# Kernel tuning notes

Hardware: AMD Instinct MI355X
Metric: run time of the kernel (lower is better)

The kernel has to match this reference:

```python
import jax, jax.numpy as jnp
import numpy as np

GAMMA = 1.0
B = 2_000_000
P = 10  # prototype_count


def setup_inputs() -> dict:
    key = jax.random.key(0)
    ks = jax.random.split(key, 17)

    def w(k, shape, scale=0.2):
        return (jax.random.normal(k, shape, dtype=jnp.float32) * scale)

    return {
        "inputs": jax.random.normal(ks[0], (B, 8), dtype=jnp.float32),
        # feature_map: Linear(8,16)
        "W_fm": w(ks[1], (8, 16)), "b_fm": w(ks[2], (16,)),
        # conv1: Linear(16,16)
        "W1": w(ks[3], (16, 16)), "b1": w(ks[4], (16,)),
        # pool1: Linear(16,12)
        "Wp1": w(ks[5], (16, 12)), "bp1": w(ks[6], (12,)),
        # conv2: Linear(12,8)
        "W2": w(ks[7], (12, 8)), "b2": w(ks[8], (8,)),
        # pool2: Linear(8,4)
        "Wp2": w(ks[9], (8, 4)), "bp2": w(ks[10], (4,)),
        # conv3: Linear(4,4)
        "W3": w(ks[11], (4, 4)), "b3": w(ks[12], (4,)),
        # prototypes in conv3 output space [P,4]
        "prototypes": jax.random.normal(ks[13], (P, 4), dtype=jnp.float32),
        # head: Linear(4+P, 1)
        "Wh": w(ks[14], (4 + P, 1)), "bh": w(ks[15], (1,)),
    }


def reference(inputs, W_fm, b_fm, W1, b1, Wp1, bp1, W2, b2, Wp2, bp2,
              W3, b3, prototypes, Wh, bh):
    # Tanh-MLP stack: 8 -> 16 -> 16 -> 12 -> 8 -> 4 -> 4
    x = jnp.tanh(inputs @ W_fm + b_fm)
    x = jnp.tanh(x @ W1 + b1)
    x = jnp.tanh(x @ Wp1 + bp1)
    x = jnp.tanh(x @ W2 + b2)
    x = jnp.tanh(x @ Wp2 + bp2)
    x = jnp.tanh(x @ W3 + b3)                      # [B, 4]
    # Vectorized RBF kernel vs prototype set (replaces per-sample Python loop):
    # ||x_i - p_j||^2 = ||x_i||^2 + ||p_j||^2 - 2 x_i . p_j
    x2 = jnp.sum(x * x, axis=-1, keepdims=True)    # [B, 1]
    p2 = jnp.sum(prototypes * prototypes, axis=-1) # [P]
    d2 = x2 + p2[None, :] - 2.0 * (x @ prototypes.T)  # [B, P]
    kernel_features = jnp.exp(-GAMMA * d2)         # [B, P]
    combined = jnp.concatenate([x, kernel_features], axis=1)  # [B, 4+P]
    return jax.nn.sigmoid(combined @ Wh + bh)      # [B, 1]
```

## Files before the change

### kernel.cpp

```cpp
#include <hip/hip_runtime.h>

#define THREADS 256
typedef float v2f __attribute__((ext_vector_type(2)));

__device__ __forceinline__ v2f tanh2(v2f x) {
    v2f xs = x * 2.885390081777927f;
    v2f e  = { __builtin_amdgcn_exp2f(xs.x),
               __builtin_amdgcn_exp2f(xs.y) };
    v2f ep = e + 1.0f;
    v2f r  = { __builtin_amdgcn_rcpf(ep.x),
               __builtin_amdgcn_rcpf(ep.y) };
    return (v2f){-2.0f, -2.0f} * r + 1.0f;
}

template<int IN, int OUT>
__device__ __forceinline__ void dense(const float* x, float* y,
                                      const float* __restrict__ W,
                                      const float* __restrict__ b) {
#pragma unroll
    for (int j = 0; j < OUT; j += 2) {
        v2f acc = { b[j], b[j + 1] };
#pragma unroll
        for (int k = 0; k < IN; ++k) {
            v2f w = { W[k * OUT + j], W[k * OUT + j + 1] };
            acc += w * x[k];
        }
        v2f t = tanh2(acc);
        y[j] = t.x; y[j + 1] = t.y;
    }
}

__global__ __launch_bounds__(THREADS) void qcnn_fused(
        const float* __restrict__ inputs,
        const float* __restrict__ W_fm, const float* __restrict__ b_fm,
        const float* __restrict__ W1,  const float* __restrict__ b1,
        const float* __restrict__ Wp1, const float* __restrict__ bp1,
        const float* __restrict__ W2,  const float* __restrict__ b2,
        const float* __restrict__ Wp2, const float* __restrict__ bp2,
        const float* __restrict__ W3,  const float* __restrict__ b3,
        const float* __restrict__ protos,
        const float* __restrict__ Wh,  const float* __restrict__ bh,
        float* __restrict__ out, int B) {
    const int tid = blockIdx.x * THREADS + threadIdx.x;
    if (tid >= B) return;

    float xa[16], xb[16];

    const float4* in4 = reinterpret_cast<const float4*>(inputs) + (size_t)tid * 2;
    float4 v0 = in4[0], v1 = in4[1];
    xa[0] = v0.x; xa[1] = v0.y; xa[2] = v0.z; xa[3] = v0.w;
    xa[4] = v1.x; xa[5] = v1.y; xa[6] = v1.z; xa[7] = v1.w;

    dense<8, 16>(xa, xb, W_fm, b_fm);
    dense<16, 16>(xb, xa, W1, b1);
    dense<16, 12>(xa, xb, Wp1, bp1);
    dense<12, 8>(xb, xa, W2, b2);
    dense<8, 4>(xa, xb, Wp2, bp2);
    dense<4, 4>(xb, xa, W3, b3);

    v2f ha = { bh[0], 0.0f };
    ha += (v2f){ xa[0], xa[1] } * (v2f){ Wh[0], Wh[1] };
    ha += (v2f){ xa[2], xa[3] } * (v2f){ Wh[2], Wh[3] };
    float acc = ha.x + ha.y;

#pragma unroll
    for (int j = 0; j < 10; j += 2) {
        v2f d2 = { 0.0f, 0.0f };
#pragma unroll
        for (int k = 0; k < 4; ++k) {
            v2f p = { protos[j * 4 + k], protos[(j + 1) * 4 + k] };
            v2f d = (v2f){ xa[k], xa[k] } - p;
            d2 += d * d;
        }
        v2f d2s = d2 * -1.4426950408889634f;
        float kf0 = __builtin_amdgcn_exp2f(d2s.x);
        float kf1 = __builtin_amdgcn_exp2f(d2s.y);
        acc = fmaf(kf0, Wh[4 + j], acc);
        acc = fmaf(kf1, Wh[5 + j], acc);
    }
    float e = __builtin_amdgcn_exp2f(acc * -1.4426950408889634f);
    out[tid] = __builtin_amdgcn_rcpf(1.0f + e);
}

extern "C" void kernel_launch(void* const* d_in, const int* in_sizes, int n_in,
                              void* d_out, int out_size, void* d_ws, size_t ws_size,
                              hipStream_t stream) {
    const float* inputs = (const float*)d_in[0];
    float* out = (float*)d_out;
    const int B = in_sizes[0] / 8;
    const int blocks = (B + THREADS - 1) / THREADS;
    qcnn_fused<<<blocks, THREADS, 0, stream>>>(
        inputs,
        (const float*)d_in[1],  (const float*)d_in[2],
        (const float*)d_in[3],  (const float*)d_in[4],
        (const float*)d_in[5],  (const float*)d_in[6],
        (const float*)d_in[7],  (const float*)d_in[8],
        (const float*)d_in[9],  (const float*)d_in[10],
        (const float*)d_in[11], (const float*)d_in[12],
        (const float*)d_in[13],
        (const float*)d_in[14], (const float*)d_in[15],
        out, B);
}
```

Before: 53.11 us.

## Process two samples per thread with packed v2f lanes across samples

Each thread now handles two batch rows (t0 and t0+gridDim*THREADS), packing the two samples into v2f lanes so every dense layer, the RBF distances and the head use packed FMA with scalar weights broadcast. The grid is halved and launch bounds request 4 waves per EU. The aim is to amortize the uniform weight loads and keep packed math fully used without pairing output columns. In exchange each thread needs more registers and has fewer threads in flight to hide memory latency.

```diff
diff --git a/kernel.cpp b/kernel.cpp
--- a/kernel.cpp
+++ b/kernel.cpp
@@ -14,23 +14,20 @@
 }
 
 template<int IN, int OUT>
-__device__ __forceinline__ void dense(const float* x, float* y,
+__device__ __forceinline__ void dense(const v2f* x, v2f* y,
                                       const float* __restrict__ W,
                                       const float* __restrict__ b) {
 #pragma unroll
-    for (int j = 0; j < OUT; j += 2) {
-        v2f acc = { b[j], b[j + 1] };
+    for (int j = 0; j < OUT; ++j) {
+        v2f acc = { b[j], b[j] };
 #pragma unroll
-        for (int k = 0; k < IN; ++k) {
-            v2f w = { W[k * OUT + j], W[k * OUT + j + 1] };
-            acc += w * x[k];
-        }
-        v2f t = tanh2(acc);
-        y[j] = t.x; y[j + 1] = t.y;
+        for (int k = 0; k < IN; ++k)
+            acc += x[k] * W[k * OUT + j];
+        y[j] = tanh2(acc);
     }
 }
 
-__global__ __launch_bounds__(THREADS) void qcnn_fused(
+__global__ __launch_bounds__(THREADS, 4) void qcnn_fused(
         const float* __restrict__ inputs,
         const float* __restrict__ W_fm, const float* __restrict__ b_fm,
         const float* __restrict__ W1,  const float* __restrict__ b1,
@@ -41,15 +38,21 @@
         const float* __restrict__ protos,
         const float* __restrict__ Wh,  const float* __restrict__ bh,
         float* __restrict__ out, int B) {
-    const int tid = blockIdx.x * THREADS + threadIdx.x;
-    if (tid >= B) return;
+    const int t0 = blockIdx.x * THREADS + threadIdx.x;
+    const int T  = gridDim.x * THREADS;
+    const int iA = t0, iB = t0 + T;
+    const bool vA = iA < B, vB = iB < B;
 
-    float xa[16], xb[16];
-
-    const float4* in4 = reinterpret_cast<const float4*>(inputs) + (size_t)tid * 2;
-    float4 v0 = in4[0], v1 = in4[1];
-    xa[0] = v0.x; xa[1] = v0.y; xa[2] = v0.z; xa[3] = v0.w;
-    xa[4] = v1.x; xa[5] = v1.y; xa[6] = v1.z; xa[7] = v1.w;
+    v2f xa[16], xb[16];
+    {
+        const float4* pa = reinterpret_cast<const float4*>(inputs) + (size_t)(vA ? iA : 0) * 2;
+        const float4* pb = reinterpret_cast<const float4*>(inputs) + (size_t)(vB ? iB : 0) * 2;
+        float4 a0 = pa[0], a1 = pa[1], b0 = pb[0], b1 = pb[1];
+        xa[0] = (v2f){a0.x, b0.x}; xa[1] = (v2f){a0.y, b0.y};
+        xa[2] = (v2f){a0.z, b0.z}; xa[3] = (v2f){a0.w, b0.w};
+        xa[4] = (v2f){a1.x, b1.x}; xa[5] = (v2f){a1.y, b1.y};
+        xa[6] = (v2f){a1.z, b1.z}; xa[7] = (v2f){a1.w, b1.w};
+    }
 
     dense<8, 16>(xa, xb, W_fm, b_fm);
     dense<16, 16>(xb, xa, W1, b1);
@@ -58,28 +61,27 @@
     dense<8, 4>(xa, xb, Wp2, bp2);
     dense<4, 4>(xb, xa, W3, b3);
 
-    v2f ha = { bh[0], 0.0f };
-    ha += (v2f){ xa[0], xa[1] } * (v2f){ Wh[0], Wh[1] };
-    ha += (v2f){ xa[2], xa[3] } * (v2f){ Wh[2], Wh[3] };
-    float acc = ha.x + ha.y;
-
+    v2f acc = { bh[0], bh[0] };
 #pragma unroll
-    for (int j = 0; j < 10; j += 2) {
+    for (int k = 0; k < 4; ++k) acc += xa[k] * Wh[k];
+#pragma unroll
+    for (int j = 0; j < 10; ++j) {
         v2f d2 = { 0.0f, 0.0f };
 #pragma unroll
         for (int k = 0; k < 4; ++k) {
-            v2f p = { protos[j * 4 + k], protos[(j + 1) * 4 + k] };
-            v2f d = (v2f){ xa[k], xa[k] } - p;
+            v2f d = xa[k] - protos[j * 4 + k];
             d2 += d * d;
         }
         v2f d2s = d2 * -1.4426950408889634f;
-        float kf0 = __builtin_amdgcn_exp2f(d2s.x);
-        float kf1 = __builtin_amdgcn_exp2f(d2s.y);
-        acc = fmaf(kf0, Wh[4 + j], acc);
-        acc = fmaf(kf1, Wh[5 + j], acc);
+        v2f kf = { __builtin_amdgcn_exp2f(d2s.x),
+                   __builtin_amdgcn_exp2f(d2s.y) };
+        acc += kf * Wh[4 + j];
     }
-    float e = __builtin_amdgcn_exp2f(acc * -1.4426950408889634f);
-    out[tid] = __builtin_amdgcn_rcpf(1.0f + e);
+    v2f as = acc * -1.4426950408889634f;
+    float eA = __builtin_amdgcn_exp2f(as.x);
+    float eB = __builtin_amdgcn_exp2f(as.y);
+    if (vA) out[iA] = __builtin_amdgcn_rcpf(1.0f + eA);
+    if (vB) out[iB] = __builtin_amdgcn_rcpf(1.0f + eB);
 }
 
 extern "C" void kernel_launch(void* const* d_in, const int* in_sizes, int n_in,
@@ -88,7 +90,7 @@
     const float* inputs = (const float*)d_in[0];
     float* out = (float*)d_out;
     const int B = in_sizes[0] / 8;
-    const int blocks = (B + THREADS - 1) / THREADS;
+    const int blocks = (B + THREADS * 2 - 1) / (THREADS * 2);
     qcnn_fused<<<blocks, THREADS, 0, stream>>>(
         inputs,
         (const float*)d_in[1],  (const float*)d_in[2],
```

Result: slower. 195.7 us (+268.5%).

## Use packed fp16 dot-product (v_dot2) for MLP layers with prepacked half weights

Applied to the files above, without the earlier changes.

Adds a tiny pre-kernel that converts the six MLP weight matrices into transposed packed half2 words in the workspace. The main kernel converts activations to half2 and accumulates each output with fdot2 (two multiply-adds per instruction, fp32 accumulate), which halves the FMA count in the compute-bound MLP. In exchange it costs fp16 rounding of weights and activations, per-layer float-to-half conversions, and an extra kernel launch per call.

```diff
diff --git a/kernel.cpp b/kernel.cpp
--- a/kernel.cpp
+++ b/kernel.cpp
@@ -1,4 +1,6 @@
 #include <hip/hip_runtime.h>
+#include <hip/hip_fp16.h>
+#include <stdint.h>
 
 #define THREADS 256
 typedef float v2f __attribute__((ext_vector_type(2)));
@@ -13,33 +15,64 @@
     return (v2f){-2.0f, -2.0f} * r + 1.0f;
 }
 
+__device__ __forceinline__ float fdot2u(uint32_t a, uint32_t b, float c) {
+#if __has_builtin(__builtin_amdgcn_fdot2)
+    typedef _Float16 h2 __attribute__((ext_vector_type(2)));
+    return __builtin_amdgcn_fdot2(__builtin_bit_cast(h2, a),
+                                  __builtin_bit_cast(h2, b), c, false);
+#else
+    __half2 ha = __builtin_bit_cast(__half2, a), hb = __builtin_bit_cast(__half2, b);
+    return c + __half2float(ha.x) * __half2float(hb.x)
+             + __half2float(ha.y) * __half2float(hb.y);
+#endif
+}
+
 template<int IN, int OUT>
-__device__ __forceinline__ void dense(const float* x, float* y,
-                                      const float* __restrict__ W,
-                                      const float* __restrict__ b) {
+__device__ __forceinline__ void dense_h(const float* x, float* y,
+                                        const uint32_t* __restrict__ wq,
+                                        const float* __restrict__ b) {
+    uint32_t hx[IN / 2];
+#pragma unroll
+    for (int p = 0; p < IN / 2; ++p)
+        hx[p] = __builtin_bit_cast(uint32_t, __floats2half2_rn(x[2 * p], x[2 * p + 1]));
 #pragma unroll
     for (int j = 0; j < OUT; j += 2) {
-        v2f acc = { b[j], b[j + 1] };
+        float a0 = b[j], a1 = b[j + 1];
 #pragma unroll
-        for (int k = 0; k < IN; ++k) {
-            v2f w = { W[k * OUT + j], W[k * OUT + j + 1] };
-            acc += w * x[k];
+        for (int p = 0; p < IN / 2; ++p) {
+            a0 = fdot2u(hx[p], wq[j * (IN / 2) + p], a0);
+            a1 = fdot2u(hx[p], wq[(j + 1) * (IN / 2) + p], a1);
         }
-        v2f t = tanh2(acc);
+        v2f t = tanh2((v2f){a0, a1});
         y[j] = t.x; y[j + 1] = t.y;
     }
 }
 
+__global__ void pack_weights(const float* __restrict__ W_fm, const float* __restrict__ W1,
+                             const float* __restrict__ Wp1, const float* __restrict__ W2,
+                             const float* __restrict__ Wp2, const float* __restrict__ W3,
+                             uint32_t* __restrict__ ws) {
+    int i = blockIdx.x * blockDim.x + threadIdx.x;
+    const float* W; int j, kp, stride, base;
+    if      (i < 64)  { int t = i;       j = t >> 2; kp = t & 3; W = W_fm; stride = 16; base = 0; }
+    else if (i < 192) { int t = i - 64;  j = t >> 3; kp = t & 7; W = W1;  stride = 16; base = 64; }
+    else if (i < 288) { int t = i - 192; j = t >> 3; kp = t & 7; W = Wp1; stride = 12; base = 192; }
+    else if (i < 336) { int t = i - 288; j = t / 6;  kp = t % 6; W = W2;  stride = 8;  base = 288; }
+    else if (i < 352) { int t = i - 336; j = t >> 2; kp = t & 3; W = Wp2; stride = 4;  base = 336; }
+    else if (i < 360) { int t = i - 352; j = t >> 1; kp = t & 1; W = W3;  stride = 4;  base = 352; }
+    else return;
+    ws[i] = __builtin_bit_cast(uint32_t,
+        __floats2half2_rn(W[(2 * kp) * stride + j], W[(2 * kp + 1) * stride + j]));
+}
+
 __global__ __launch_bounds__(THREADS) void qcnn_fused(
         const float* __restrict__ inputs,
-        const float* __restrict__ W_fm, const float* __restrict__ b_fm,
-        const float* __restrict__ W1,  const float* __restrict__ b1,
-        const float* __restrict__ Wp1, const float* __restrict__ bp1,
-        const float* __restrict__ W2,  const float* __restrict__ b2,
-        const float* __restrict__ Wp2, const float* __restrict__ bp2,
-        const float* __restrict__ W3,  const float* __restrict__ b3,
+        const uint32_t* __restrict__ wq,
+        const float* __restrict__ b_fm, const float* __restrict__ b1,
+        const float* __restrict__ bp1,  const float* __restrict__ b2,
+        const float* __restrict__ bp2,  const float* __restrict__ b3,
         const float* __restrict__ protos,
-        const float* __restrict__ Wh,  const float* __restrict__ bh,
+        const float* __restrict__ Wh,   const float* __restrict__ bh,
         float* __restrict__ out, int B) {
     const int tid = blockIdx.x * THREADS + threadIdx.x;
     if (tid >= B) return;
@@ -51,12 +84,12 @@
     xa[0] = v0.x; xa[1] = v0.y; xa[2] = v0.z; xa[3] = v0.w;
     xa[4] = v1.x; xa[5] = v1.y; xa[6] = v1.z; xa[7] = v1.w;
 
-    dense<8, 16>(xa, xb, W_fm, b_fm);
-    dense<16, 16>(xb, xa, W1, b1);
-    dense<16, 12>(xa, xb, Wp1, bp1);
-    dense<12, 8>(xb, xa, W2, b2);
-    dense<8, 4>(xa, xb, Wp2, bp2);
-    dense<4, 4>(xb, xa, W3, b3);
+    dense_h<8, 16>(xa, xb, wq + 0,   b_fm);
+    dense_h<16, 16>(xb, xa, wq + 64,  b1);
+    dense_h<16, 12>(xa, xb, wq + 192, bp1);
+    dense_h<12, 8>(xb, xa, wq + 288, b2);
+    dense_h<8, 4>(xa, xb, wq + 336, bp2);
+    dense_h<4, 4>(xb, xa, wq + 352, b3);
 
     v2f ha = { bh[0], 0.0f };
     ha += (v2f){ xa[0], xa[1] } * (v2f){ Wh[0], Wh[1] };
@@ -88,15 +121,19 @@
     const float* inputs = (const float*)d_in[0];
     float* out = (float*)d_out;
     const int B = in_sizes[0] / 8;
+
+    uint32_t* wq = (uint32_t*)d_ws;
+    pack_weights<<<1, 512, 0, stream>>>(
+        (const float*)d_in[1],  (const float*)d_in[3],  (const float*)d_in[5],
+        (const float*)d_in[7],  (const float*)d_in[9],  (const float*)d_in[11],
+        wq);
+
     const int blocks = (B + THREADS - 1) / THREADS;
     qcnn_fused<<<blocks, THREADS, 0, stream>>>(
-        inputs,
-        (const float*)d_in[1],  (const float*)d_in[2],
-        (const float*)d_in[3],  (const float*)d_in[4],
-        (const float*)d_in[5],  (const float*)d_in[6],
-        (const float*)d_in[7],  (const float*)d_in[8],
-        (const float*)d_in[9],  (const float*)d_in[10],
-        (const float*)d_in[11], (const float*)d_in[12],
+        inputs, wq,
+        (const float*)d_in[2],  (const float*)d_in[4],
+        (const float*)d_in[6],  (const float*)d_in[8],
+        (const float*)d_in[10], (const float*)d_in[12],
         (const float*)d_in[13],
         (const float*)d_in[14], (const float*)d_in[15],
         out, B);
```

Result: slower. 58.92 us (+10.9%).
